# Kernel tuning notes

Hardware: AMD Instinct MI355X
Metric: run time of the kernel (lower is better)

Reference implementation:

```python
import jax, jax.numpy as jnp
import numpy as np

N_NODES = 100000
N_EDGES = 1600000
D_FEAT = 128
HIDDEN = 128
N_CLASSES = 10
N_GRAPHS = 64


def setup_inputs() -> dict:
    key = jax.random.key(0)
    ks = jax.random.split(key, 8)
    x = jax.random.normal(ks[0], (N_NODES, D_FEAT), dtype=jnp.float32)
    edge_index = jax.random.randint(ks[1], (2, N_EDGES), 0, N_NODES, dtype=jnp.int64)
    batch = jnp.sort(jax.random.randint(ks[2], (N_NODES,), 0, N_GRAPHS, dtype=jnp.int64))
    # GraphConv params: lin_rel (weight+bias) applied to aggregated neighbors,
    # lin_root (weight only) applied to self features. Final classifier lin.
    s = 1.0 / np.sqrt(D_FEAT)
    w_rel = jax.random.uniform(ks[3], (HIDDEN, D_FEAT), jnp.float32, -s, s)
    b_rel = jax.random.uniform(ks[4], (HIDDEN,), jnp.float32, -s, s)
    w_root = jax.random.uniform(ks[5], (HIDDEN, D_FEAT), jnp.float32, -s, s)
    sl = 1.0 / np.sqrt(HIDDEN)
    w_lin = jax.random.uniform(ks[6], (N_CLASSES, HIDDEN), jnp.float32, -sl, sl)
    b_lin = jax.random.uniform(ks[7], (N_CLASSES,), jnp.float32, -sl, sl)
    return {"x": x, "edge_index": edge_index, "batch": batch,
            "w_rel": w_rel, "b_rel": b_rel, "w_root": w_root,
            "w_lin": w_lin, "b_lin": b_lin}


def reference(x, edge_index, batch, w_rel, b_rel, w_root, w_lin, b_lin):
    src, dst = edge_index[0], edge_index[1]
    # GraphConv(aggr='add'): gather source features, scatter-add to targets
    agg = jax.ops.segment_sum(x[src], dst, num_segments=N_NODES)  # [N, F]
    h = agg @ w_rel.T + b_rel + x @ w_root.T                      # [N, H]
    # global_mean_pool over graph ids
    summed = jax.ops.segment_sum(h, batch, num_segments=N_GRAPHS)            # [G, H]
    counts = jax.ops.segment_sum(jnp.ones((N_NODES,), h.dtype), batch,
                                 num_segments=N_GRAPHS)                       # [G]
    pooled = summed / jnp.maximum(counts, 1.0)[:, None]
    # final classifier (dropout==0 so it is a no-op)
    return pooled @ w_lin.T + b_lin                                # [G, C]
```

## Files before the change

kernel.cpp:

```cpp
#include <hip/hip_runtime.h>

#define N_NODES  100000
#define N_EDGES  1600000
#define D        128
#define NG       64
#define NC       10
#define NBMAX    512
#define TILE     64
#define EPT      8
#define ABLK     196
#define NBUCK    391
#define BCAP     8192
#define CBLK2    98
#define CIW      68
#define XSW      130

typedef unsigned int uint;
typedef unsigned short ushort;
typedef unsigned long long ull;
typedef short bhalf8 __attribute__((ext_vector_type(8)));
typedef float f32x4  __attribute__((ext_vector_type(4)));

#define MFMA_BF16 __builtin_amdgcn_mfma_f32_16x16x32_bf16

#define OFF_COUNTS 391
#define ZERO_U32   512
#define BDATA_U32  (NBUCK * (BCAP / 2))
#define OFF_CNT    (ZERO_U32 + BDATA_U32)

static_assert(ABLK * 1024 * EPT >= N_EDGES, "edge coverage");
static_assert(NBUCK * 256 >= N_NODES, "bucket coverage");

__global__ __launch_bounds__(256) void fill_kernel(uint* __restrict__ p)
{
    const int i = blockIdx.x * 256 + threadIdx.x;
    if (i < ZERO_U32) p[i] = 0u;
}

__global__ __launch_bounds__(1024) void bucket_kernel(
    const int* __restrict__ ei, const int* __restrict__ batch,
    uint* __restrict__ tail, int* __restrict__ counts,
    ushort* __restrict__ bdata)
{
    const int b = blockIdx.x;
    if (b < ABLK) {
        __shared__ uint hs[NBUCK];
        __shared__ uint he[NBUCK];
        const int t = threadIdx.x;
        for (int i = t; i < NBUCK; i += 1024) hs[i] = 0u;
        __syncthreads();

        const int e0 = b * (1024 * EPT) + t * EPT;
        uint er[EPT];
        int  s[EPT], dn[EPT];
        bool v[EPT];
        if (e0 + EPT <= N_EDGES) {
            const int4 a0 = *reinterpret_cast<const int4*>(ei + e0);
            const int4 a1 = *reinterpret_cast<const int4*>(ei + e0 + 4);
            const int4 b0 = *reinterpret_cast<const int4*>(ei + N_EDGES + e0);
            const int4 b1 = *reinterpret_cast<const int4*>(ei + N_EDGES + e0 + 4);
            s[0]=a0.x; s[1]=a0.y; s[2]=a0.z; s[3]=a0.w;
            s[4]=a1.x; s[5]=a1.y; s[6]=a1.z; s[7]=a1.w;
            dn[0]=b0.x; dn[1]=b0.y; dn[2]=b0.z; dn[3]=b0.w;
            dn[4]=b1.x; dn[5]=b1.y; dn[6]=b1.z; dn[7]=b1.w;
            #pragma unroll
            for (int i = 0; i < EPT; ++i) v[i] = true;
        } else {
            #pragma unroll
            for (int i = 0; i < EPT; ++i) {
                v[i] = (e0 + i) < N_EDGES;
                s[i]  = v[i] ? ei[e0 + i] : 0;
                dn[i] = v[i] ? ei[N_EDGES + e0 + i] : 0;
            }
        }
        #pragma unroll
        for (int i = 0; i < EPT; ++i) {
            if (v[i]) {
                const uint g = (uint)batch[dn[i]];
                const uint k = (uint)s[i] >> 8;
                er[i] = (k << 16) | (((uint)s[i] & 255u) << 6) | g;
                atomicAdd(&hs[k], 1u);
            } else er[i] = 0xFFFFFFFFu;
        }
        __syncthreads();
        if (t < NBUCK) {
            const uint c = hs[t];
            uint r = 0u, a = 0u;
            if (c) { a = (c + 31u) & ~31u; r = atomicAdd(&tail[t], a); }
            hs[t] = r;
            he[t] = r + a;
        }
        __syncthreads();
        #pragma unroll
        for (int i = 0; i < EPT; ++i) {
            if (er[i] != 0xFFFFFFFFu) {
                const uint k = er[i] >> 16;
                const uint pos = atomicAdd(&hs[k], 1u);
                if (pos < BCAP)
                    bdata[(size_t)k * BCAP + pos] = (ushort)(er[i] & 0xFFFFu);
            }
        }
        __syncthreads();
        if (t < NBUCK) {
            uint p = hs[t];
            uint e = he[t];
            if (e > BCAP) e = BCAP;
            for (; p < e; ++p) bdata[(size_t)t * BCAP + p] = 0xFFFFu;
        }
    } else {
        const int n = (b - ABLK) * 1024 + threadIdx.x;
        if (n >= N_NODES) return;
        const int lane = threadIdx.x & 63;
        const int g = batch[n];
        const bool lead = (n == 0) || (lane == 0) || (batch[n - 1] != g);
        const ull bl = __ballot(lead);
        if (lead) {
            const ull higher = (lane == 63) ? 0ull : (bl >> (lane + 1));
            int end = higher ? (lane + 1 + (__ffsll(higher) - 1)) : 64;
            const int wb = n - lane;
            int nv = N_NODES - wb; if (nv > 64) nv = 64;
            if (end > nv) end = nv;
            atomicAdd(&counts[g], end - lane);
        }
    }
}

__global__ __launch_bounds__(256) void hist_kernel(
    const uint* __restrict__ tail, const ushort* __restrict__ bdata,
    uint* __restrict__ cnt)
{
    __shared__ uint h2[256 * NG];
    const int k = blockIdx.x;
    const int t = threadIdx.x;
    {
        const uint4 z = {0u, 0u, 0u, 0u};
        uint4* h4 = reinterpret_cast<uint4*>(h2);
        for (int i = t; i < 256 * NG / 4; i += 256) h4[i] = z;
    }
    __syncthreads();

    uint n = tail[k]; if (n > BCAP) n = BCAP;
    const ushort* __restrict__ bp = bdata + (size_t)k * BCAP;
    for (uint i = t; i < n; i += 256) {
        const uint r = bp[i];
        if (r != 0xFFFFu) atomicAdd(&h2[r], 1u);
    }
    __syncthreads();

    const int node0 = k * 256;
    const int nrows = min(256, N_NODES - node0);
    for (int j = t; j < nrows * 16; j += 256) {
        const int node = j >> 4, g4 = j & 15;
        const uint* hp = &h2[node * NG + g4 * 4];
        const uint w = (hp[0] & 255u) | ((hp[1] & 255u) << 8)
                     | ((hp[2] & 255u) << 16) | ((hp[3] & 255u) << 24);
        cnt[(size_t)(node0 + node) * 16 + g4] = w;
    }
}

__device__ __forceinline__ uint packbf(float f)
{
    const uint u  = __float_as_uint(f);
    const uint hb = (u + 0x7FFFu + ((u >> 16) & 1u)) >> 16;
    const float hf = __uint_as_float(hb << 16);
    const uint ul = __float_as_uint(f - hf);
    const uint lb = (ul + 0x7FFFu + ((ul >> 16) & 1u)) >> 16;
    return hb | (lb << 16);
}

__global__ __launch_bounds__(1024, 8) void gemm_kernel(
    const float* __restrict__ x, const uint* __restrict__ cnt,
    const int* __restrict__ batch,
    float* __restrict__ partA, float* __restrict__ partX, int NBe)
{
    __shared__ uint xsp[TILE * XSW];
    __shared__ uint ci[NG * CIW];

    const int t   = threadIdx.x;
    const int l   = t & 63;
    const int w   = t >> 6;
    const int mt  = w & 3;
    const int nt0 = (w >> 2) << 1;
    const int lr  = l & 15;
    const int lh  = l >> 4;

    f32x4 aA0 = {0,0,0,0}, aA1 = {0,0,0,0};
    f32x4 aX0 = {0,0,0,0}, aX1 = {0,0,0,0};

    const int ntiles = (N_NODES + TILE - 1) / TILE;
    for (int tb = blockIdx.x; tb < ntiles; tb += NBe) {
        const int base = tb * TILE;
        const int nvalid = min(TILE, N_NODES - base);

        #pragma unroll
        for (int k = 0; k < 2; ++k) {
            const int f4i = t + k * 1024;
            const int n = f4i >> 5, c4 = f4i & 31;
            float4 v = make_float4(0.f, 0.f, 0.f, 0.f);
            if (n < nvalid)
                v = *reinterpret_cast<const float4*>(x + (size_t)(base + n) * D + c4 * 4);
            uint2 p01, p23;
            p01.x = packbf(v.x); p01.y = packbf(v.y);
            p23.x = packbf(v.z); p23.y = packbf(v.w);
            uint* dst = xsp + n * XSW + c4 * 4;
            *reinterpret_cast<uint2*>(dst)     = p01;
            *reinterpret_cast<uint2*>(dst + 2) = p23;
        }
        {
            const int node = t >> 4, slot = t & 15;
            uint cv = 0u; int gb = -1;
            if (node < nvalid) {
                cv = cnt[(size_t)(base + node) * 16 + slot];
                gb = batch[base + node];
            }
            #pragma unroll
            for (int j = 0; j < 4; ++j) {
                const int g = slot * 4 + j;
                const uint c = (cv >> (8 * j)) & 255u;
                uint val = __float_as_uint((float)c) >> 16;
                if (gb == g) val |= 0x3F800000u;
                ci[g * CIW + node] = val;
            }
        }
        __syncthreads();

        #pragma unroll
        for (int kc = 0; kc < 2; ++kc) {
            const int k0 = kc * 32;
            const uint* cip = ci + (mt * 16 + lr) * CIW + k0 + lh * 8;
            const uint4 ca = *reinterpret_cast<const uint4*>(cip);
            const uint4 cb = *reinterpret_cast<const uint4*>(cip + 4);
            bhalf8 acnt, aind;
            acnt[0]=(short)ca.x; aind[0]=(short)(ca.x>>16);
            acnt[1]=(short)ca.y; aind[1]=(short)(ca.y>>16);
            acnt[2]=(short)ca.z; aind[2]=(short)(ca.z>>16);
            acnt[3]=(short)ca.w; aind[3]=(short)(ca.w>>16);
            acnt[4]=(short)cb.x; aind[4]=(short)(cb.x>>16);
            acnt[5]=(short)cb.y; aind[5]=(short)(cb.y>>16);
            acnt[6]=(short)cb.z; aind[6]=(short)(cb.z>>16);
            acnt[7]=(short)cb.w; aind[7]=(short)(cb.w>>16);

            const uint* xb = xsp + (k0 + lh * 8) * XSW + lr;
            {
                const uint* xp = xb + nt0 * 16;
                const uint r0=xp[0],      r1=xp[XSW],   r2=xp[2*XSW], r3=xp[3*XSW],
                           r4=xp[4*XSW],  r5=xp[5*XSW], r6=xp[6*XSW], r7=xp[7*XSW];
                bhalf8 bh, bl;
                bh[0]=(short)r0; bl[0]=(short)(r0>>16);
                bh[1]=(short)r1; bl[1]=(short)(r1>>16);
                bh[2]=(short)r2; bl[2]=(short)(r2>>16);
                bh[3]=(short)r3; bl[3]=(short)(r3>>16);
                bh[4]=(short)r4; bl[4]=(short)(r4>>16);
                bh[5]=(short)r5; bl[5]=(short)(r5>>16);
                bh[6]=(short)r6; bl[6]=(short)(r6>>16);
                bh[7]=(short)r7; bl[7]=(short)(r7>>16);
                aA0 = MFMA_BF16(acnt, bh, aA0, 0, 0, 0);
                aA0 = MFMA_BF16(acnt, bl, aA0, 0, 0, 0);
                aX0 = MFMA_BF16(aind, bh, aX0, 0, 0, 0);
                aX0 = MFMA_BF16(aind, bl, aX0, 0, 0, 0);
            }
            {
                const uint* xp = xb + (nt0 + 1) * 16;
                const uint r0=xp[0],      r1=xp[XSW],   r2=xp[2*XSW], r3=xp[3*XSW],
                           r4=xp[4*XSW],  r5=xp[5*XSW], r6=xp[6*XSW], r7=xp[7*XSW];
                bhalf8 bh, bl;
                bh[0]=(short)r0; bl[0]=(short)(r0>>16);
                bh[1]=(short)r1; bl[1]=(short)(r1>>16);
                bh[2]=(short)r2; bl[2]=(short)(r2>>16);
                bh[3]=(short)r3; bl[3]=(short)(r3>>16);
                bh[4]=(short)r4; bl[4]=(short)(r4>>16);
                bh[5]=(short)r5; bl[5]=(short)(r5>>16);
                bh[6]=(short)r6; bl[6]=(short)(r6>>16);
                bh[7]=(short)r7; bl[7]=(short)(r7>>16);
                aA1 = MFMA_BF16(acnt, bh, aA1, 0, 0, 0);
                aA1 = MFMA_BF16(acnt, bl, aA1, 0, 0, 0);
                aX1 = MFMA_BF16(aind, bh, aX1, 0, 0, 0);
                aX1 = MFMA_BF16(aind, bl, aX1, 0, 0, 0);
            }
        }
        __syncthreads();
    }

    float* pa = partA + (size_t)blockIdx.x * (NG * D);
    float* px = partX + (size_t)blockIdx.x * (NG * D);
    #pragma unroll
    for (int r = 0; r < 4; ++r) {
        const int row = mt * 16 + lh * 4 + r;
        pa[row * D + nt0 * 16 + lr]       = aA0[r];
        pa[row * D + (nt0 + 1) * 16 + lr] = aA1[r];
        px[row * D + nt0 * 16 + lr]       = aX0[r];
        px[row * D + (nt0 + 1) * 16 + lr] = aX1[r];
    }
}

__global__ __launch_bounds__(256) void reduce1_kernel(
    const float* __restrict__ partA, const float* __restrict__ partX,
    float* __restrict__ tmp2, int NBe)
{
    const int cb = blockIdx.x & 63;
    const int pc = blockIdx.x >> 6;
    const int c  = cb * 256 + threadIdx.x;
    const float* __restrict__ srcp =
        (c < NG * D) ? (partA + c) : (partX + (c - NG * D));
    const int chunk = (NBe + 3) >> 2;
    const int p0 = pc * chunk;
    int p1 = p0 + chunk; if (p1 > NBe) p1 = NBe;
    float s = 0.f;
    #pragma unroll 8
    for (int p = p0; p < p1; ++p) s += srcp[(size_t)p * (NG * D)];
    tmp2[pc * (2 * NG * D) + c] = s;
}

__global__ __launch_bounds__(128) void final_kernel(
    const float* __restrict__ tmp2, const int* __restrict__ counts,
    const float* __restrict__ w_rel, const float* __restrict__ b_rel,
    const float* __restrict__ w_root,
    const float* __restrict__ w_lin, const float* __restrict__ b_lin,
    float* __restrict__ out)
{
    const int g = blockIdx.x;
    const int t = threadIdx.x;

    __shared__ float agg_s[D], x_s[D], p_s[D];
    float a = 0.f, xsum = 0.f;
    #pragma unroll
    for (int j = 0; j < 4; ++j) {
        a    += tmp2[j * (2 * NG * D) + g * D + t];
        xsum += tmp2[j * (2 * NG * D) + NG * D + g * D + t];
    }
    agg_s[t] = a; x_s[t] = xsum;
    __syncthreads();

    const float cn = (float)counts[g];
    float hj = b_rel[t] * cn;
    const float* __restrict__ wr = w_rel  + (size_t)t * D;
    const float* __restrict__ wo = w_root + (size_t)t * D;
    #pragma unroll 8
    for (int d0 = 0; d0 < D; ++d0) hj += agg_s[d0] * wr[d0] + x_s[d0] * wo[d0];
    p_s[t] = hj / fmaxf(cn, 1.f);
    __syncthreads();

    if (t < NC) {
        const float* __restrict__ wl = w_lin + (size_t)t * D;
        float o = b_lin[t];
        #pragma unroll 8
        for (int d0 = 0; d0 < D; ++d0) o += p_s[d0] * wl[d0];
        out[g * NC + t] = o;
    }
}

extern "C" void kernel_launch(void* const* d_in, const int* in_sizes, int n_in,
                              void* d_out, int out_size, void* d_ws, size_t ws_size,
                              hipStream_t stream)
{
    const float* x      = (const float*)d_in[0];
    const int*   ei     = (const int*)  d_in[1];
    const int*   batch  = (const int*)  d_in[2];
    const float* w_rel  = (const float*)d_in[3];
    const float* b_rel  = (const float*)d_in[4];
    const float* w_root = (const float*)d_in[5];
    const float* w_lin  = (const float*)d_in[6];
    const float* b_lin  = (const float*)d_in[7];
    float* out = (float*)d_out;

    uint*   tail   = (uint*)d_ws;
    int*    counts = (int*)(tail + OFF_COUNTS);
    ushort* bdata  = (ushort*)(tail + ZERO_U32);
    uint*   cnt    = tail + OFF_CNT;
    float*  partA  = (float*)(cnt + (size_t)N_NODES * 16);

    const size_t availf = ws_size / sizeof(float);
    const size_t headf  = OFF_CNT + (size_t)N_NODES * 16;
    const size_t tmp2f  = 4 * (size_t)(2 * NG * D);
    int NBe = NBMAX;
    if (headf + tmp2f + (size_t)NBe * 2 * NG * D > availf) {
        long long rem = (long long)availf - (long long)(headf + tmp2f);
        long long nb  = rem / (2 * NG * D);
        NBe = (nb < 1) ? 1 : (int)nb;
    }
    float* partX = partA + (size_t)NBe * NG * D;
    float* tmp2  = partX + (size_t)NBe * NG * D;

    fill_kernel<<<2, 256, 0, stream>>>(tail);
    bucket_kernel<<<ABLK + CBLK2, 1024, 0, stream>>>(ei, batch, tail, counts, bdata);
    hist_kernel<<<NBUCK, 256, 0, stream>>>(tail, bdata, cnt);
    gemm_kernel<<<NBe, 1024, 0, stream>>>(x, cnt, batch, partA, partX, NBe);
    reduce1_kernel<<<256, 256, 0, stream>>>(partA, partX, tmp2, NBe);
    final_kernel<<<NG, 128, 0, stream>>>(tmp2, counts,
                                         w_rel, b_rel, w_root, w_lin, b_lin, out);
}
```

Before: 83.68 us.

## Fuse per-node graph-count histogram into GEMM kernel, drop hist kernel

Removes the separate histogram kernel and its per-node packed count array. Each GEMM tile now builds its own 64x64 node-by-graph histogram in shared memory by scanning the bucket records of its 256-node bucket and keeping only those for its quarter. This saves one launch and the global write and read of the count array. In exchange, every bucket's records are scanned four times (once per tile), the loop gains an extra shared-memory zeroing pass and a barrier, and shared memory per block grows.

```diff
diff --git a/kernel.cpp b/kernel.cpp
--- a/kernel.cpp
+++ b/kernel.cpp
@@ -26,7 +26,6 @@
 #define OFF_COUNTS 391
 #define ZERO_U32   512
 #define BDATA_U32  (NBUCK * (BCAP / 2))
-#define OFF_CNT    (ZERO_U32 + BDATA_U32)
 
 static_assert(ABLK * 1024 * EPT >= N_EDGES, "edge coverage");
 static_assert(NBUCK * 256 >= N_NODES, "bucket coverage");
@@ -125,39 +124,6 @@
     }
 }
 
-__global__ __launch_bounds__(256) void hist_kernel(
-    const uint* __restrict__ tail, const ushort* __restrict__ bdata,
-    uint* __restrict__ cnt)
-{
-    __shared__ uint h2[256 * NG];
-    const int k = blockIdx.x;
-    const int t = threadIdx.x;
-    {
-        const uint4 z = {0u, 0u, 0u, 0u};
-        uint4* h4 = reinterpret_cast<uint4*>(h2);
-        for (int i = t; i < 256 * NG / 4; i += 256) h4[i] = z;
-    }
-    __syncthreads();
-
-    uint n = tail[k]; if (n > BCAP) n = BCAP;
-    const ushort* __restrict__ bp = bdata + (size_t)k * BCAP;
-    for (uint i = t; i < n; i += 256) {
-        const uint r = bp[i];
-        if (r != 0xFFFFu) atomicAdd(&h2[r], 1u);
-    }
-    __syncthreads();
-
-    const int node0 = k * 256;
-    const int nrows = min(256, N_NODES - node0);
-    for (int j = t; j < nrows * 16; j += 256) {
-        const int node = j >> 4, g4 = j & 15;
-        const uint* hp = &h2[node * NG + g4 * 4];
-        const uint w = (hp[0] & 255u) | ((hp[1] & 255u) << 8)
-                     | ((hp[2] & 255u) << 16) | ((hp[3] & 255u) << 24);
-        cnt[(size_t)(node0 + node) * 16 + g4] = w;
-    }
-}
-
 __device__ __forceinline__ uint packbf(float f)
 {
     const uint u  = __float_as_uint(f);
@@ -169,12 +135,14 @@
 }
 
 __global__ __launch_bounds__(1024, 8) void gemm_kernel(
-    const float* __restrict__ x, const uint* __restrict__ cnt,
+    const float* __restrict__ x,
+    const uint* __restrict__ tail, const ushort* __restrict__ bdata,
     const int* __restrict__ batch,
     float* __restrict__ partA, float* __restrict__ partX, int NBe)
 {
     __shared__ uint xsp[TILE * XSW];
     __shared__ uint ci[NG * CIW];
+    __shared__ uint h[TILE * NG];
 
     const int t   = threadIdx.x;
     const int l   = t & 63;
@@ -189,9 +157,13 @@
 
     const int ntiles = (N_NODES + TILE - 1) / TILE;
     for (int tb = blockIdx.x; tb < ntiles; tb += NBe) {
-        const int base = tb * TILE;
+        const int base   = tb * TILE;
         const int nvalid = min(TILE, N_NODES - base);
-
+        const int bk     = tb >> 2;
+        const uint qsel  = (uint)(tb & 3);
+
+        #pragma unroll
+        for (int k = 0; k < 4; ++k) h[t + k * 1024] = 0u;
         #pragma unroll
         for (int k = 0; k < 2; ++k) {
             const int f4i = t + k * 1024;
@@ -206,18 +178,28 @@
             *reinterpret_cast<uint2*>(dst)     = p01;
             *reinterpret_cast<uint2*>(dst + 2) = p23;
         }
+        __syncthreads();
+
+        {
+            uint nrec = tail[bk]; if (nrec > BCAP) nrec = BCAP;
+            const ushort* __restrict__ bp = bdata + (size_t)bk * BCAP;
+            for (uint i = (uint)t; i < nrec; i += 1024u) {
+                const uint r = bp[i];
+                if (r != 0xFFFFu && ((r >> 12) & 3u) == qsel)
+                    atomicAdd(&h[((r >> 6) & 63u) * NG + (r & 63u)], 1u);
+            }
+        }
+        __syncthreads();
+
         {
             const int node = t >> 4, slot = t & 15;
-            uint cv = 0u; int gb = -1;
-            if (node < nvalid) {
-                cv = cnt[(size_t)(base + node) * 16 + slot];
-                gb = batch[base + node];
-            }
+            const int gb = (node < nvalid) ? batch[base + node] : -1;
+            const uint4 hv = *reinterpret_cast<const uint4*>(&h[node * NG + slot * 4]);
+            const uint hc[4] = {hv.x, hv.y, hv.z, hv.w};
             #pragma unroll
             for (int j = 0; j < 4; ++j) {
                 const int g = slot * 4 + j;
-                const uint c = (cv >> (8 * j)) & 255u;
-                uint val = __float_as_uint((float)c) >> 16;
+                uint val = __float_as_uint((float)hc[j]) >> 16;
                 if (gb == g) val |= 0x3F800000u;
                 ci[g * CIW + node] = val;
             }
@@ -366,11 +348,10 @@
     uint*   tail   = (uint*)d_ws;
     int*    counts = (int*)(tail + OFF_COUNTS);
     ushort* bdata  = (ushort*)(tail + ZERO_U32);
-    uint*   cnt    = tail + OFF_CNT;
-    float*  partA  = (float*)(cnt + (size_t)N_NODES * 16);
+    float*  partA  = (float*)(tail + ZERO_U32 + BDATA_U32);
 
     const size_t availf = ws_size / sizeof(float);
-    const size_t headf  = OFF_CNT + (size_t)N_NODES * 16;
+    const size_t headf  = ZERO_U32 + BDATA_U32;
     const size_t tmp2f  = 4 * (size_t)(2 * NG * D);
     int NBe = NBMAX;
     if (headf + tmp2f + (size_t)NBe * 2 * NG * D > availf) {
@@ -383,8 +364,7 @@
 
     fill_kernel<<<2, 256, 0, stream>>>(tail);
     bucket_kernel<<<ABLK + CBLK2, 1024, 0, stream>>>(ei, batch, tail, counts, bdata);
-    hist_kernel<<<NBUCK, 256, 0, stream>>>(tail, bdata, cnt);
-    gemm_kernel<<<NBe, 1024, 0, stream>>>(x, cnt, batch, partA, partX, NBe);
+    gemm_kernel<<<NBe, 1024, 0, stream>>>(x, tail, bdata, batch, partA, partX, NBe);
     reduce1_kernel<<<256, 256, 0, stream>>>(partA, partX, tmp2, NBe);
     final_kernel<<<NG, 128, 0, stream>>>(tmp2, counts,
                                          w_rel, b_rel, w_root, w_lin, b_lin, out);
```

Measured after the change: 78.92 us. 5.7% less time.
